# Kernel optimization log

Measured on AMD Instinct MI355X. Metric: run time of the kernel, lower is better.

Reference implementation:

```python
import jax, jax.numpy as jnp
import numpy as np
import math

SEQ_LEN = 64
INPUT_DIM = 1
HID = 1024
BATCH = 1024  # must equal HID due to the module's bias-broadcast over columns


def setup_inputs() -> dict:
    key = jax.random.key(0)
    ks = jax.random.split(key, 12)
    stdv = 1.0 / math.sqrt(HID)
    x = jax.random.normal(ks[0], (BATCH, SEQ_LEN), dtype=jnp.float32)
    def w(k):
        return stdv * jax.random.normal(k, (HID, HID + INPUT_DIM), dtype=jnp.float32)
    def b(k):
        return stdv * jax.random.normal(k, (HID,), dtype=jnp.float32)
    return {
        "x": x,
        "w_g": w(ks[1]), "b_g": b(ks[2]),
        "w_i": w(ks[3]), "b_i": b(ks[4]),
        "w_f": w(ks[5]), "b_f": b(ks[6]),
        "w_o": w(ks[7]), "b_o": b(ks[8]),
        "w_p": stdv * jax.random.normal(ks[9], (HID, HID), dtype=jnp.float32),
        "b_p": stdv * jax.random.normal(ks[10], (HID,), dtype=jnp.float32),
    }


def _lstm_forward(x, w_g, b_g, w_i, b_i, w_f, b_f, w_o, b_o, w_p, b_p):
    B, T = x.shape
    H = w_g.shape[0]
    # Fuse the 4 gate GEMMs into one stacked GEMM (identical math).
    w_all = jnp.concatenate([w_g, w_i, w_f, w_o], axis=0)  # [4H, H+1]

    def step(carry, x_t):
        h, c = carry                                   # [H, B] each
        hx = jnp.concatenate([x_t[None, :], h], axis=0)  # [1+H, B]
        z = w_all @ hx                                 # [4H, B]
        zg, zi, zf, zo = jnp.split(z, 4, axis=0)
        # NOTE: biases broadcast over the LAST axis (columns), exactly as in
        # the torch source (`[H,B] + [H]`), which requires B == H.
        g = jnp.tanh(zg + b_g)
        i = jax.nn.sigmoid(zi + b_i)
        f = jax.nn.sigmoid(zf + b_f)
        o = jax.nn.sigmoid(zo + b_o)
        c2 = g * i + c * f
        h2 = jnp.tanh(c2) * o
        return (h2, c2), None

    h0 = jnp.zeros((H, B), dtype=x.dtype)
    c0 = jnp.zeros((H, B), dtype=x.dtype)
    (hT, _), _ = jax.lax.scan(step, (h0, c0), x.T)  # scan over time: x.T is [T, B]
    p = w_p @ hT + b_p[:, None]                     # [H, B]
    return p.T                                      # [B, H]


def reference(x, w_g, b_g, w_i, b_i, w_f, b_f, w_o, b_o, w_p, b_p):
    return _lstm_forward(x, w_g, b_g, w_i, b_i, w_f, b_f, w_o, b_o, w_p, b_p)
```

## Files before the change

kernel.cpp:

```cpp
#include <hip/hip_runtime.h>


typedef _Float16 f16;
typedef __attribute__((ext_vector_type(8))) _Float16 f16x8;
typedef __attribute__((ext_vector_type(4))) float f32x4;

typedef const __attribute__((address_space(1))) unsigned char* gbl_ptr_t;
typedef __attribute__((address_space(3))) unsigned char* lds_ptr_t;

__device__ __forceinline__ float fsig(float z) {
  return 1.0f / (1.0f + __expf(-z));
}
__device__ __forceinline__ float ftanh(float z) {
  float a = fabsf(z);
  float e = __expf(-2.0f * a);
  float t = (1.0f - e) / (1.0f + e);
  return z < 0.0f ? -t : t;
}

__global__ __launch_bounds__(256) void k_prep(
    const float* __restrict__ wg, const float* __restrict__ wi,
    const float* __restrict__ wf, const float* __restrict__ wo,
    const float* __restrict__ wp,
    f16* __restrict__ Wf, float* __restrict__ w0,
    f16* __restrict__ WPf) {
  const int NW = 4 * 1024 * 1025;
  const int NP = 1024 * 1024;
  int i = blockIdx.x * blockDim.x + threadIdx.x;
  const int stride = gridDim.x * blockDim.x;
  for (; i < NW + NP; i += stride) {
    if (i < NW) {
      const int gate = i / (1024 * 1025);
      const int rem = i - gate * (1024 * 1025);
      const int r = rem / 1025;
      const int k = rem - r * 1025;
      const float* w = gate == 0 ? wg : gate == 1 ? wi : gate == 2 ? wf : wo;
      const float v = w[rem];
      if (k == 0) {
        w0[gate * 1024 + r] = v;
      } else {
        Wf[(gate * 1024 + r) * 1024 + (k - 1)] = (f16)v;
      }
    } else {
      WPf[i - NW] = (f16)wp[i - NW];
    }
  }
}

__global__ __launch_bounds__(512) void k_step(
    const f16* __restrict__ Wf,
    const float* __restrict__ w0,
    const float* __restrict__ x,
    const float* __restrict__ bg, const float* __restrict__ bi,
    const float* __restrict__ bff, const float* __restrict__ bo,
    const f16* __restrict__ Hin, f16* __restrict__ Hout,
    float* __restrict__ c, int t) {
  __shared__ alignas(16) unsigned char smem[98304];
  const int tid = threadIdx.x;
  const int wid = tid >> 6;
  const int lane = tid & 63;
  const int gate = wid >> 1;
  const int wn = wid & 1;
  const int hr0 = (blockIdx.x & 31) * 32;
  const int b0 = (blockIdx.x >> 5) * 128;
  const unsigned SETB = 32768;

  long aoffb[2], boffb[2];
  int ldso[2];
#pragma unroll
  for (int s = 0; s < 2; ++s) {
    const int ch = s * 512 + tid;
    const int row = ch >> 3;
    const int sl = ch & 7;
    const int sg = sl ^ (row & 7);
    const int gt = row >> 5, rin = row & 31;
    aoffb[s] = ((long)(gt * 1024 + hr0 + rin) << 10) + sg * 8;
    boffb[s] = ((long)(b0 + row) << 10) + sg * 8;
    ldso[s] = ch * 16;
  }

  f32x4 acc[2][4];
#pragma unroll
  for (int m = 0; m < 2; ++m)
#pragma unroll
    for (int n = 0; n < 4; ++n) acc[m][n] = (f32x4){0.f, 0.f, 0.f, 0.f};

#pragma unroll
  for (int p = 0; p < 2; ++p) {
    const unsigned nb = p * SETB;
    const int k0 = p << 6;
#pragma unroll
    for (int s = 0; s < 2; ++s) {
      __builtin_amdgcn_global_load_lds((gbl_ptr_t)(const void*)(Wf + aoffb[s] + k0),
                                       (lds_ptr_t)(void*)(smem + nb + ldso[s]), 16, 0, 0);
      __builtin_amdgcn_global_load_lds((gbl_ptr_t)(const void*)(Hin + boffb[s] + k0),
                                       (lds_ptr_t)(void*)(smem + nb + 16384 + ldso[s]), 16, 0, 0);
    }
  }
  asm volatile("s_waitcnt vmcnt(4)" ::: "memory");
  __builtin_amdgcn_s_barrier();
  asm volatile("" ::: "memory");

#pragma unroll
  for (int kt = 0; kt < 16; ++kt) {
    const unsigned pb = (unsigned)(kt % 3) * SETB;
    if (kt < 14) {
      const unsigned nb = (unsigned)((kt + 2) % 3) * SETB;
      const int k0 = (kt + 2) << 6;
#pragma unroll
      for (int s = 0; s < 2; ++s) {
        __builtin_amdgcn_global_load_lds((gbl_ptr_t)(const void*)(Wf + aoffb[s] + k0),
                                         (lds_ptr_t)(void*)(smem + nb + ldso[s]), 16, 0, 0);
        __builtin_amdgcn_global_load_lds((gbl_ptr_t)(const void*)(Hin + boffb[s] + k0),
                                         (lds_ptr_t)(void*)(smem + nb + 16384 + ldso[s]), 16, 0, 0);
      }
    }
    __builtin_amdgcn_s_setprio(1);
#pragma unroll
    for (int ks = 0; ks < 2; ++ks) {
      const int slot = (ks << 2) + (lane >> 4);
      f16x8 aF[2];
#pragma unroll
      for (int m = 0; m < 2; ++m) {
        const int tra = gate * 32 + m * 16 + (lane & 15);
        const int offa = tra * 128 + ((slot ^ (tra & 7)) << 4);
        aF[m] = *(const f16x8*)(smem + pb + offa);
      }
#pragma unroll
      for (int n = 0; n < 4; ++n) {
        const int trb = wn * 64 + n * 16 + (lane & 15);
        const int offb = trb * 128 + ((slot ^ (trb & 7)) << 4);
        const f16x8 bF = *(const f16x8*)(smem + pb + 16384 + offb);
#pragma unroll
        for (int m = 0; m < 2; ++m) {
          acc[m][n] = __builtin_amdgcn_mfma_f32_16x16x32_f16(aF[m], bF, acc[m][n], 0, 0, 0);
        }
      }
    }
    __builtin_amdgcn_s_setprio(0);
    if (kt < 14) {
      asm volatile("s_waitcnt vmcnt(4)" ::: "memory");
    } else if (kt == 14) {
      asm volatile("s_waitcnt vmcnt(0)" ::: "memory");
    }
    if (kt < 15) {
      __builtin_amdgcn_s_barrier();
      asm volatile("" ::: "memory");
    }
  }
  __syncthreads();

  float* zl = (float*)smem;
#pragma unroll
  for (int n = 0; n < 4; ++n) {
    const int b = wn * 64 + n * 16 + (lane & 15);
#pragma unroll
    for (int m = 0; m < 2; ++m) {
#pragma unroll
      for (int j = 0; j < 4; ++j) {
        const int r = m * 16 + (lane >> 4) * 4 + j;
        const int rs = (r ^ ((b & 7) << 2)) ^ ((b >> 3) & 1);
        zl[gate * 4096 + b * 32 + rs] = acc[m][n][j];
      }
    }
  }
  __syncthreads();
  for (int q = 0; q < 8; ++q) {
    const int idx = q * 512 + tid;
    const int r = idx & 31, bb = idx >> 5;
    const int rs = (r ^ ((bb & 7) << 2)) ^ ((bb >> 3) & 1);
    const int gb = b0 + bb;
    const int gr = hr0 + r;
    float zg = zl[bb * 32 + rs];
    float zi = zl[4096 + bb * 32 + rs];
    float zf = zl[8192 + bb * 32 + rs];
    float zo = zl[12288 + bb * 32 + rs];
    const float xv = x[gb * 64 + t];
    zg += w0[gr] * xv + bg[gb];
    zi += w0[1024 + gr] * xv + bi[gb];
    zf += w0[2048 + gr] * xv + bff[gb];
    zo += w0[3072 + gr] * xv + bo[gb];
    const float g = ftanh(zg), ii = fsig(zi), ff = fsig(zf), oo = fsig(zo);
    const long ci = (long)gb * 1024 + gr;
    const float c2 = g * ii + c[ci] * ff;
    c[ci] = c2;
    const float h2 = ftanh(c2) * oo;
    Hout[ci] = (f16)h2;
  }
}

__global__ __launch_bounds__(256) void k_proj(
    const f16* __restrict__ H, const f16* __restrict__ WPf,
    const float* __restrict__ bp, float* __restrict__ out) {
  __shared__ alignas(16) unsigned char smem[32768];
  const int tid = threadIdx.x;
  const int wid = tid >> 6;
  const int lane = tid & 63;
  const int b0 = (blockIdx.x >> 3) * 128;
  const int r0 = (blockIdx.x & 7) * 128;

  f32x4 acc[2][8];
#pragma unroll
  for (int m = 0; m < 2; ++m)
#pragma unroll
    for (int n = 0; n < 8; ++n) acc[m][n] = (f32x4){0.f, 0.f, 0.f, 0.f};

  for (int kt = 0; kt < 16; ++kt) {
    const int k0 = kt << 6;
    __syncthreads();
#pragma unroll
    for (int j = 0; j < 4; ++j) {
      const int i = wid * 4 + j;
      const int ch = i * 64 + lane;
      const int row = ch >> 3;
      const int sl = ch & 7;
      const int sg = sl ^ (row & 7);
      const long aoff = ((long)(b0 + row) << 10) + k0 + sg * 8;
      const long boff = ((long)(r0 + row) << 10) + k0 + sg * 8;
      __builtin_amdgcn_global_load_lds((gbl_ptr_t)(const void*)(H + aoff),
                                       (lds_ptr_t)(void*)(smem + i * 1024), 16, 0, 0);
      __builtin_amdgcn_global_load_lds((gbl_ptr_t)(const void*)(WPf + boff),
                                       (lds_ptr_t)(void*)(smem + 16384 + i * 1024), 16, 0, 0);
    }
    __syncthreads();
#pragma unroll
    for (int ks = 0; ks < 2; ++ks) {
      const int slot = (ks << 2) + (lane >> 4);
      f16x8 aF[2];
#pragma unroll
      for (int m = 0; m < 2; ++m) {
        const int tr = wid * 32 + m * 16 + (lane & 15);
        const int off = tr * 128 + ((slot ^ (tr & 7)) << 4);
        aF[m] = *(const f16x8*)(smem + off);
      }
#pragma unroll
      for (int n = 0; n < 8; ++n) {
        const int tr = n * 16 + (lane & 15);
        const int off = tr * 128 + ((slot ^ (tr & 7)) << 4);
        const f16x8 bF = *(const f16x8*)(smem + 16384 + off);
#pragma unroll
        for (int m = 0; m < 2; ++m) {
          acc[m][n] = __builtin_amdgcn_mfma_f32_16x16x32_f16(aF[m], bF, acc[m][n], 0, 0, 0);
        }
      }
    }
  }
#pragma unroll
  for (int n = 0; n < 8; ++n) {
    const int rr = r0 + n * 16 + (lane & 15);
    const float bpv = bp[rr];
#pragma unroll
    for (int m = 0; m < 2; ++m) {
#pragma unroll
      for (int j = 0; j < 4; ++j) {
        const int bbb = b0 + wid * 32 + m * 16 + (lane >> 4) * 4 + j;
        out[(long)bbb * 1024 + rr] = acc[m][n][j] + bpv;
      }
    }
  }
}

extern "C" void kernel_launch(void* const* d_in, const int* in_sizes, int n_in,
                              void* d_out, int out_size, void* d_ws, size_t ws_size,
                              hipStream_t stream) {
  (void)in_sizes; (void)n_in; (void)out_size; (void)ws_size;
  const float* x  = (const float*)d_in[0];
  const float* wg = (const float*)d_in[1];
  const float* bg = (const float*)d_in[2];
  const float* wi = (const float*)d_in[3];
  const float* bi = (const float*)d_in[4];
  const float* wf = (const float*)d_in[5];
  const float* bf = (const float*)d_in[6];
  const float* wo = (const float*)d_in[7];
  const float* bo = (const float*)d_in[8];
  const float* wp = (const float*)d_in[9];
  const float* bp = (const float*)d_in[10];

  char* ws = (char*)d_ws;
  size_t off = 0;
  auto alloc = [&](size_t bytes) {
    char* p = ws + off;
    off += (bytes + 255) & ~(size_t)255;
    return p;
  };
  f16*   Wf  = (f16*)alloc(8388608);
  f16*   WPf = (f16*)alloc(2097152);
  float* w0  = (float*)alloc(16384);
  f16*   h0  = (f16*)alloc(2097152);
  f16*   h1  = (f16*)alloc(2097152);
  float* c   = (float*)alloc(4194304);

  hipMemsetAsync(h0, 0, 2097152, stream);
  hipMemsetAsync(c, 0, 4194304, stream);

  k_prep<<<2048, 256, 0, stream>>>(wg, wi, wf, wo, wp, Wf, w0, WPf);

  for (int t = 0; t < 64; ++t) {
    const f16* ih = (t & 1) ? h1 : h0;
    f16* oh = (t & 1) ? h0 : h1;
    k_step<<<256, 512, 0, stream>>>(Wf, w0, x, bg, bi, bf, bo, ih, oh, c, t);
  }
  k_proj<<<64, 256, 0, stream>>>(h0, WPf, bp, (float*)d_out);
}
```

Measured before the change: 1.134 ms.

## Load weight fragments directly to registers and double-buffer only H in LDS

The A (weight) operand is now loaded straight from global memory into registers in MFMA fragment layout, double-buffered across k-tiles, instead of being staged through LDS. Only the H operand still goes through LDS, which shrinks shared memory from 96KB to 64KB and turns the three-stage pipeline into a two-stage one. The aim is to cut LDS traffic and footprint, possibly allowing more occupancy. In exchange the per-lane global loads are strided rather than coalesced row chunks, the prefetch distance is shorter, and every k-tile now ends in a full __syncthreads rather than a tuned partial vmcnt wait.

```diff
diff --git a/kernel.cpp b/kernel.cpp
--- a/kernel.cpp
+++ b/kernel.cpp
@@ -55,7 +55,7 @@
     const float* __restrict__ bff, const float* __restrict__ bo,
     const f16* __restrict__ Hin, f16* __restrict__ Hout,
     float* __restrict__ c, int t) {
-  __shared__ alignas(16) unsigned char smem[98304];
+  __shared__ alignas(16) unsigned char smem[65536];
   const int tid = threadIdx.x;
   const int wid = tid >> 6;
   const int lane = tid & 63;
@@ -63,9 +63,8 @@
   const int wn = wid & 1;
   const int hr0 = (blockIdx.x & 31) * 32;
   const int b0 = (blockIdx.x >> 5) * 128;
-  const unsigned SETB = 32768;
-
-  long aoffb[2], boffb[2];
+
+  long boffb[2];
   int ldso[2];
 #pragma unroll
   for (int s = 0; s < 2; ++s) {
@@ -73,82 +72,72 @@
     const int row = ch >> 3;
     const int sl = ch & 7;
     const int sg = sl ^ (row & 7);
-    const int gt = row >> 5, rin = row & 31;
-    aoffb[s] = ((long)(gt * 1024 + hr0 + rin) << 10) + sg * 8;
     boffb[s] = ((long)(b0 + row) << 10) + sg * 8;
     ldso[s] = ch * 16;
   }
 
+  int aoff[2][2];
+#pragma unroll
+  for (int m = 0; m < 2; ++m)
+#pragma unroll
+    for (int ks = 0; ks < 2; ++ks)
+      aoff[m][ks] = (gate * 1024 + hr0 + m * 16 + (lane & 15)) * 1024 +
+                    ks * 32 + (lane >> 4) * 8;
+
   f32x4 acc[2][4];
 #pragma unroll
   for (int m = 0; m < 2; ++m)
 #pragma unroll
     for (int n = 0; n < 4; ++n) acc[m][n] = (f32x4){0.f, 0.f, 0.f, 0.f};
 
-#pragma unroll
-  for (int p = 0; p < 2; ++p) {
-    const unsigned nb = p * SETB;
-    const int k0 = p << 6;
-#pragma unroll
-    for (int s = 0; s < 2; ++s) {
-      __builtin_amdgcn_global_load_lds((gbl_ptr_t)(const void*)(Wf + aoffb[s] + k0),
-                                       (lds_ptr_t)(void*)(smem + nb + ldso[s]), 16, 0, 0);
-      __builtin_amdgcn_global_load_lds((gbl_ptr_t)(const void*)(Hin + boffb[s] + k0),
-                                       (lds_ptr_t)(void*)(smem + nb + 16384 + ldso[s]), 16, 0, 0);
-    }
-  }
-  asm volatile("s_waitcnt vmcnt(4)" ::: "memory");
-  __builtin_amdgcn_s_barrier();
-  asm volatile("" ::: "memory");
+  f16x8 Abuf[2][2][2];
+
+#pragma unroll
+  for (int s = 0; s < 2; ++s)
+    __builtin_amdgcn_global_load_lds((gbl_ptr_t)(const void*)(Hin + boffb[s]),
+                                     (lds_ptr_t)(void*)(smem + ldso[s]), 16, 0, 0);
+#pragma unroll
+  for (int m = 0; m < 2; ++m)
+#pragma unroll
+    for (int ks = 0; ks < 2; ++ks)
+      Abuf[0][m][ks] = *(const f16x8*)(Wf + aoff[m][ks]);
+  __syncthreads();
 
 #pragma unroll
   for (int kt = 0; kt < 16; ++kt) {
-    const unsigned pb = (unsigned)(kt % 3) * SETB;
-    if (kt < 14) {
-      const unsigned nb = (unsigned)((kt + 2) % 3) * SETB;
-      const int k0 = (kt + 2) << 6;
-#pragma unroll
-      for (int s = 0; s < 2; ++s) {
-        __builtin_amdgcn_global_load_lds((gbl_ptr_t)(const void*)(Wf + aoffb[s] + k0),
+    const unsigned pb = (kt & 1) * 16384;
+    if (kt < 15) {
+      const unsigned nb = ((kt + 1) & 1) * 16384;
+      const int k0 = (kt + 1) << 6;
+#pragma unroll
+      for (int s = 0; s < 2; ++s)
+        __builtin_amdgcn_global_load_lds((gbl_ptr_t)(const void*)(Hin + boffb[s] + k0),
                                          (lds_ptr_t)(void*)(smem + nb + ldso[s]), 16, 0, 0);
-        __builtin_amdgcn_global_load_lds((gbl_ptr_t)(const void*)(Hin + boffb[s] + k0),
-                                         (lds_ptr_t)(void*)(smem + nb + 16384 + ldso[s]), 16, 0, 0);
-      }
+#pragma unroll
+      for (int m = 0; m < 2; ++m)
+#pragma unroll
+        for (int ks = 0; ks < 2; ++ks)
+          Abuf[(kt + 1) & 1][m][ks] = *(const f16x8*)(Wf + aoff[m][ks] + k0);
     }
     __builtin_amdgcn_s_setprio(1);
 #pragma unroll
     for (int ks = 0; ks < 2; ++ks) {
       const int slot = (ks << 2) + (lane >> 4);
-      f16x8 aF[2];
-#pragma unroll
-      for (int m = 0; m < 2; ++m) {
-        const int tra = gate * 32 + m * 16 + (lane & 15);
-        const int offa = tra * 128 + ((slot ^ (tra & 7)) << 4);
-        aF[m] = *(const f16x8*)(smem + pb + offa);
-      }
 #pragma unroll
       for (int n = 0; n < 4; ++n) {
         const int trb = wn * 64 + n * 16 + (lane & 15);
         const int offb = trb * 128 + ((slot ^ (trb & 7)) << 4);
-        const f16x8 bF = *(const f16x8*)(smem + pb + 16384 + offb);
+        const f16x8 bF = *(const f16x8*)(smem + pb + offb);
 #pragma unroll
         for (int m = 0; m < 2; ++m) {
-          acc[m][n] = __builtin_amdgcn_mfma_f32_16x16x32_f16(aF[m], bF, acc[m][n], 0, 0, 0);
+          acc[m][n] = __builtin_amdgcn_mfma_f32_16x16x32_f16(Abuf[kt & 1][m][ks], bF,
+                                                             acc[m][n], 0, 0, 0);
         }
       }
     }
     __builtin_amdgcn_s_setprio(0);
-    if (kt < 14) {
-      asm volatile("s_waitcnt vmcnt(4)" ::: "memory");
-    } else if (kt == 14) {
-      asm volatile("s_waitcnt vmcnt(0)" ::: "memory");
-    }
-    if (kt < 15) {
-      __builtin_amdgcn_s_barrier();
-      asm volatile("" ::: "memory");
-    }
-  }
-  __syncthreads();
+    __syncthreads();
+  }
 
   float* zl = (float*)smem;
 #pragma unroll
```

After: 1.923 ms. 1.7x slower.
